# Performance work log

Hardware: AMD Instinct MI355X
Metric: run time of the kernel (lower is better)

The kernel has to match this reference:

```python
import jax, jax.numpy as jnp
import numpy as np
import math

N_HEADS = 12
EPS = 1e-5

def _layernorm(x, w, b):
    # torch .var() is unbiased (ddof=1)
    mean = jnp.mean(x, axis=-1, keepdims=True)
    var = jnp.var(x, axis=-1, keepdims=True, ddof=1)
    return (x - mean) / jnp.sqrt(var + EPS) * w + b

def _gelu_tanh(x):
    c = math.sqrt(2.0 / math.pi)
    return 0.5 * x * (1.0 + jnp.tanh(c * (x + 0.044715 * x * x * x)))

def setup_inputs() -> dict:
    key = jax.random.key(0)
    ks = jax.random.split(key, 6)
    B, T, C = 4, 2048, 768
    s = 0.02
    return {
        "x": jax.random.normal(ks[0], (B, T, C), jnp.float32),
        "ln1_w": jnp.ones((C,), jnp.float32),
        "ln1_b": jnp.zeros((C,), jnp.float32),
        "c_attn_w": jax.random.normal(ks[1], (C, 3 * C), jnp.float32) * s,
        "c_attn_b": jnp.zeros((3 * C,), jnp.float32),
        "c_proj_w": jax.random.normal(ks[2], (C, C), jnp.float32) * s,
        "c_proj_b": jnp.zeros((C,), jnp.float32),
        "ln2_w": jnp.ones((C,), jnp.float32),
        "ln2_b": jnp.zeros((C,), jnp.float32),
        "fc_w": jax.random.normal(ks[3], (C, 4 * C), jnp.float32) * s,
        "fc_b": jnp.zeros((4 * C,), jnp.float32),
        "mproj_w": jax.random.normal(ks[4], (4 * C, C), jnp.float32) * s,
        "mproj_b": jnp.zeros((C,), jnp.float32),
    }

def _attention(x, c_attn_w, c_attn_b, c_proj_w, c_proj_b):
    B, T, C = x.shape
    H = N_HEADS
    D = C // H
    qkv = x @ c_attn_w + c_attn_b  # [B,T,3C]
    q, k, v = jnp.split(qkv, 3, axis=-1)
    q = q.reshape(B, T, H, D).transpose(0, 2, 1, 3)  # [B,H,T,D]
    k = k.reshape(B, T, H, D).transpose(0, 2, 1, 3)
    v = v.reshape(B, T, H, D).transpose(0, 2, 1, 3)
    scores = jnp.einsum("bhqd,bhkd->bhqk", q, k) * (D ** -0.5)  # [B,H,T,T]
    causal = jnp.tril(jnp.ones((T, T), bool))
    scores = jnp.where(causal[None, None], scores, jnp.float32(-jnp.inf))
    attn = jax.nn.softmax(scores, axis=-1)
    out = jnp.einsum("bhqk,bhkd->bhqd", attn, v)  # [B,H,T,D]
    out = out.transpose(0, 2, 1, 3).reshape(B, T, C)
    return out @ c_proj_w + c_proj_b

def reference(x, ln1_w, ln1_b, c_attn_w, c_attn_b, c_proj_w, c_proj_b,
              ln2_w, ln2_b, fc_w, fc_b, mproj_w, mproj_b):
    x = x + _attention(_layernorm(x, ln1_w, ln1_b), c_attn_w, c_attn_b, c_proj_w, c_proj_b)
    h = _gelu_tanh(_layernorm(x, ln2_w, ln2_b) @ fc_w + fc_b)
    return x + h @ mproj_w + mproj_b
```

## Files before the change

### kernel.cpp

```cpp
#include <hip/hip_runtime.h>
#include <hip/hip_bf16.h>
#include <cstdint>

#define BF __hip_bfloat16

typedef __bf16 v8bf __attribute__((ext_vector_type(8)));
typedef float  v4f  __attribute__((ext_vector_type(4)));

__device__ __forceinline__ float tof(BF v) { return __bfloat162float(v); }
__device__ __forceinline__ BF    tob(float v) { return __float2bfloat16(v); }
__device__ __forceinline__ float ldf(float v) { return v; }
__device__ __forceinline__ float ldf(BF v) { return tof(v); }
__device__ __forceinline__ void stv(float* p, float v) { *p = v; }
__device__ __forceinline__ void stv(BF* p, float v) { *p = tob(v); }

__device__ __forceinline__ v4f mfma16(v8bf a, v8bf b, v4f c) {
  return __builtin_amdgcn_mfma_f32_16x16x32_bf16(a, b, c, 0, 0, 0);
}

__device__ __forceinline__ void async16(const BF* g, BF* l) {
  __builtin_amdgcn_global_load_lds((const __attribute__((address_space(1))) void*)g,
                                   (__attribute__((address_space(3))) void*)l, 16, 0, 0);
}

__global__ __launch_bounds__(256) void transpose_k(const float* __restrict__ in,
                                                   BF* __restrict__ out, int R, int C) {
  __shared__ BF t[64][65];
  int tid = threadIdx.x;
  int c0 = blockIdx.x * 64, r0 = blockIdx.y * 64;
#pragma unroll
  for (int i = 0; i < 16; ++i) {
    int idx = i * 256 + tid;
    int rr = idx >> 6, cc = idx & 63;
    t[rr][cc] = tob(in[(size_t)(r0 + rr) * C + c0 + cc]);
  }
  __syncthreads();
#pragma unroll
  for (int i = 0; i < 16; ++i) {
    int idx = i * 256 + tid;
    int rr = idx >> 6, cc = idx & 63;
    out[(size_t)(c0 + rr) * R + r0 + cc] = t[cc][rr];
  }
}

__global__ __launch_bounds__(256) void vtrans_k(const BF* __restrict__ qkv,
                                                BF* __restrict__ vT) {
  __shared__ BF t[64][65];
  int tid = threadIdx.x;
  int t0 = blockIdx.x * 64;
  int bh = blockIdx.y;
  int b = bh / 12, h = bh % 12;
  const BF* src = qkv + (size_t)(b * 2048 + t0) * 2304 + 1536 + h * 64;
#pragma unroll
  for (int i = 0; i < 16; ++i) {
    int idx = i * 256 + tid;
    int rr = idx >> 6, cc = idx & 63;
    t[rr][cc] = src[(size_t)rr * 2304 + cc];
  }
  __syncthreads();
  BF* dst = vT + (size_t)bh * 64 * 2048 + t0;
#pragma unroll
  for (int i = 0; i < 16; ++i) {
    int idx = i * 256 + tid;
    int rr = idx >> 6, cc = idx & 63;
    dst[(size_t)rr * 2048 + cc] = t[cc][rr];
  }
}

template <typename TX>
__global__ __launch_bounds__(256) void ln_k(const TX* __restrict__ x,
                                            const float* __restrict__ w,
                                            const float* __restrict__ bia,
                                            BF* __restrict__ y) {
  int row = blockIdx.x, tid = threadIdx.x;
  const TX* xr = x + (size_t)row * 768;
  float v0 = ldf(xr[tid]), v1 = ldf(xr[tid + 256]), v2 = ldf(xr[tid + 512]);
  float s1 = v0 + v1 + v2;
  float s2 = v0 * v0 + v1 * v1 + v2 * v2;
#pragma unroll
  for (int m = 32; m; m >>= 1) { s1 += __shfl_xor(s1, m); s2 += __shfl_xor(s2, m); }
  __shared__ float rs[4][2];
  int wv = tid >> 6;
  if ((tid & 63) == 0) { rs[wv][0] = s1; rs[wv][1] = s2; }
  __syncthreads();
  s1 = rs[0][0] + rs[1][0] + rs[2][0] + rs[3][0];
  s2 = rs[0][1] + rs[1][1] + rs[2][1] + rs[3][1];
  float mean = s1 * (1.0f / 768.0f);
  float var = fmaxf((s2 - s1 * mean) * (1.0f / 767.0f), 0.0f);
  float rstd = rsqrtf(var + 1e-5f);
  BF* yr = y + (size_t)row * 768;
  yr[tid]       = tob((v0 - mean) * rstd * w[tid]       + bia[tid]);
  yr[tid + 256] = tob((v1 - mean) * rstd * w[tid + 256] + bia[tid + 256]);
  yr[tid + 512] = tob((v2 - mean) * rstd * w[tid + 512] + bia[tid + 512]);
}

__device__ __forceinline__ float gelu_f(float x) {
  float u = 0.7978845608028654f * (x + 0.044715f * x * x * x);
  float e = exp2f(2.8853900817779268f * u);
  return 0.5f * x * (1.0f + (1.0f - 2.0f / (e + 1.0f)));
}

template <int BN, int ACT, bool RESID, typename TR, typename TO>
__global__ __launch_bounds__(256) void gemm_bt_k(
    const BF* __restrict__ A, const BF* __restrict__ Bt, const float* __restrict__ bias,
    const TR* __restrict__ resid, TO* __restrict__ out, int M, int N, int K) {
  constexpr int NW = BN / 32;
  __shared__ __align__(16) BF As[2][128 * 64];
  __shared__ __align__(16) BF Bs[2][BN * 64];
  const int tid = threadIdx.x;
  const int w = tid >> 6, lane = tid & 63;
  const int quad = lane >> 4, l16 = lane & 15;
  const int gx = gridDim.x;
  const int nwg = gx * gridDim.y;
  const int lid = blockIdx.y * gx + blockIdx.x;
  const int swz = (lid & 7) * (nwg >> 3) + (lid >> 3);
  const int m0 = (swz / gx) * 128, n0 = (swz % gx) * BN;
  const int wm = (w >> 1) * 64, wn = (w & 1) * (BN / 2);
  const int sr = lane >> 3;
  const int sc = ((lane & 7) ^ sr) * 8;

  v4f acc[4][NW];
#pragma unroll
  for (int i = 0; i < 4; ++i)
#pragma unroll
    for (int j = 0; j < NW; ++j) acc[i][j] = (v4f){0.f, 0.f, 0.f, 0.f};

  auto stage = [&](int bsel, int k0) {
#pragma unroll
    for (int i = 0; i < 4; ++i) {
      int r0 = w * 32 + i * 8;
      async16(A + (size_t)(m0 + r0 + sr) * K + k0 + sc, &As[bsel][r0 * 64]);
    }
    if (BN == 128) {
#pragma unroll
      for (int i = 0; i < 4; ++i) {
        int r0 = w * 32 + i * 8;
        async16(Bt + (size_t)(n0 + r0 + sr) * K + k0 + sc, &Bs[bsel][r0 * 64]);
      }
    } else {
#pragma unroll
      for (int i = 0; i < 2; ++i) {
        int r0 = w * 16 + i * 8;
        async16(Bt + (size_t)(n0 + r0 + sr) * K + k0 + sc, &Bs[bsel][r0 * 64]);
      }
    }
  };

  const int nkt = K >> 6;
  stage(0, 0);
  __syncthreads();
  for (int kt = 0; kt < nkt; ++kt) {
    const int cur = kt & 1;
    if (kt + 1 < nkt) stage(cur ^ 1, (kt + 1) << 6);
#pragma unroll
    for (int kk = 0; kk < 2; ++kk) {
      v8bf af[4], bfv[NW];
#pragma unroll
      for (int mi = 0; mi < 4; ++mi) {
        int row = wm + mi * 16 + l16;
        af[mi] = *(const v8bf*)&As[cur][row * 64 + (((kk * 4 + quad) ^ (row & 7)) * 8)];
      }
#pragma unroll
      for (int nj = 0; nj < NW; ++nj) {
        int row = wn + nj * 16 + l16;
        bfv[nj] = *(const v8bf*)&Bs[cur][row * 64 + (((kk * 4 + quad) ^ (row & 7)) * 8)];
      }
      __builtin_amdgcn_s_setprio(1);
#pragma unroll
      for (int mi = 0; mi < 4; ++mi)
#pragma unroll
        for (int nj = 0; nj < NW; ++nj)
          acc[mi][nj] = mfma16(af[mi], bfv[nj], acc[mi][nj]);
      __builtin_amdgcn_s_setprio(0);
    }
    __syncthreads();
  }

#pragma unroll
  for (int nj = 0; nj < NW; ++nj) {
    int col = n0 + wn + nj * 16 + l16;
    float bv = bias[col];
#pragma unroll
    for (int mi = 0; mi < 4; ++mi) {
      v4f c = acc[mi][nj];
#pragma unroll
      for (int r = 0; r < 4; ++r) {
        int row = m0 + wm + mi * 16 + quad * 4 + r;
        float v = c[r] + bv;
        if (RESID) v += ldf(resid[(size_t)row * N + col]);
        if (ACT == 1) v = gelu_f(v);
        stv(&out[(size_t)row * N + col], v);
      }
    }
  }
}

__global__ __launch_bounds__(256) void attn_k(const BF* __restrict__ qkv,
                                              const BF* __restrict__ vT,
                                              BF* __restrict__ out) {
  __shared__ __align__(16) BF Ks[64 * 64];
  __shared__ __align__(16) BF Vs[64 * 64];
  __shared__ __align__(16) BF Ps[4][16 * 64];
  const int tid = threadIdx.x;
  const int w = tid >> 6, lane = tid & 63;
  const int quad = lane >> 4, l16 = lane & 15;
  const int bid = blockIdx.x;
  const int qi = 31 - (bid / 48);
  const int bh = bid % 48;
  const int b = bh / 12, h = bh % 12;
  const int q0 = qi * 64;
  const int qf = q0 + w * 16;
  BF* Pw = &Ps[w][0];
  const float L2E = 1.4426950408889634f;

  auto sz = [](int r, int c) { return (r << 6) + (c ^ ((r & 7) << 3)); };

  const BF* qp = qkv + (size_t)(b * 2048 + qf + l16) * 2304 + h * 64;
  v8bf q0v = *(const v8bf*)(qp + quad * 8);
  v8bf q1v = *(const v8bf*)(qp + 32 + quad * 8);
#pragma unroll
  for (int i = 0; i < 8; ++i) {
    q0v[i] = (__bf16)(tof((BF)q0v[i]) * 0.125f);
    q1v[i] = (__bf16)(tof((BF)q1v[i]) * 0.125f);
  }
  v8bf ones;
#pragma unroll
  for (int i = 0; i < 8; ++i) ones[i] = (__bf16)1.0f;

  v4f O[4], S;
#pragma unroll
  for (int j = 0; j < 4; ++j) O[j] = (v4f){0.f, 0.f, 0.f, 0.f};
  S = (v4f){0.f, 0.f, 0.f, 0.f};

  const BF* kg = qkv + (size_t)b * 2048 * 2304 + 768 + h * 64;
  const BF* vg = vT + (size_t)bh * 64 * 2048;
  const int r0 = tid >> 3, c0 = (tid & 7) * 8;
  const int r1 = r0 + 32;
  const int nIter = qi + 1;

  v8bf nk0 = *(const v8bf*)(kg + (size_t)r0 * 2304 + c0);
  v8bf nk1 = *(const v8bf*)(kg + (size_t)r1 * 2304 + c0);
  v8bf nv0 = *(const v8bf*)(vg + (size_t)r0 * 2048 + c0);
  v8bf nv1 = *(const v8bf*)(vg + (size_t)r1 * 2048 + c0);

  for (int t = 0; t < nIter; ++t) {
    const int kt0 = t * 64;
    __syncthreads();
    *(v8bf*)&Ks[sz(r0, c0)] = nk0;
    *(v8bf*)&Ks[sz(r1, c0)] = nk1;
    *(v8bf*)&Vs[sz(r0, c0)] = nv0;
    *(v8bf*)&Vs[sz(r1, c0)] = nv1;
    __syncthreads();
    if (t + 1 < nIter) {
      const int kn = kt0 + 64;
      nk0 = *(const v8bf*)(kg + (size_t)(kn + r0) * 2304 + c0);
      nk1 = *(const v8bf*)(kg + (size_t)(kn + r1) * 2304 + c0);
      nv0 = *(const v8bf*)(vg + (size_t)r0 * 2048 + kn + c0);
      nv1 = *(const v8bf*)(vg + (size_t)r1 * 2048 + kn + c0);
    }
    v4f s[4];
    __builtin_amdgcn_s_setprio(1);
#pragma unroll
    for (int nt = 0; nt < 4; ++nt) {
      v8bf kf0 = *(const v8bf*)&Ks[sz(nt * 16 + l16, quad * 8)];
      v8bf kf1 = *(const v8bf*)&Ks[sz(nt * 16 + l16, 32 + quad * 8)];
      s[nt] = mfma16(q1v, kf1, mfma16(q0v, kf0, (v4f){0.f, 0.f, 0.f, 0.f}));
    }
    __builtin_amdgcn_s_setprio(0);
    if (t < qi) {
#pragma unroll
      for (int nt = 0; nt < 4; ++nt)
#pragma unroll
        for (int r = 0; r < 4; ++r)
          Pw[sz(quad * 4 + r, nt * 16 + l16)] = tob(exp2f(s[nt][r] * L2E));
    } else {
#pragma unroll
      for (int nt = 0; nt < 4; ++nt) {
        int key = kt0 + nt * 16 + l16;
#pragma unroll
        for (int r = 0; r < 4; ++r) {
          int qrow = qf + quad * 4 + r;
          float p = (key <= qrow) ? exp2f(s[nt][r] * L2E) : 0.f;
          Pw[sz(quad * 4 + r, nt * 16 + l16)] = tob(p);
        }
      }
    }
    asm volatile("s_waitcnt lgkmcnt(0)" ::: "memory");
    v8bf p0 = *(const v8bf*)&Pw[sz(l16, quad * 8)];
    v8bf p1 = *(const v8bf*)&Pw[sz(l16, 32 + quad * 8)];
    __builtin_amdgcn_s_setprio(1);
#pragma unroll
    for (int j = 0; j < 4; ++j) {
      v8bf vf0 = *(const v8bf*)&Vs[sz(j * 16 + l16, quad * 8)];
      v8bf vf1 = *(const v8bf*)&Vs[sz(j * 16 + l16, 32 + quad * 8)];
      O[j] = mfma16(p1, vf1, mfma16(p0, vf0, O[j]));
    }
    S = mfma16(p1, ones, mfma16(p0, ones, S));
    __builtin_amdgcn_s_setprio(0);
  }

#pragma unroll
  for (int r = 0; r < 4; ++r) {
    float inv = 1.0f / S[r];
    int row = b * 2048 + qf + quad * 4 + r;
    BF* op = out + (size_t)row * 768 + h * 64 + l16;
#pragma unroll
    for (int j = 0; j < 4; ++j) op[j * 16] = tob(O[j][r] * inv);
  }
}

extern "C" void kernel_launch(void* const* d_in, const int* in_sizes, int n_in,
                              void* d_out, int out_size, void* d_ws, size_t ws_size,
                              hipStream_t stream) {
  const float* x        = (const float*)d_in[0];
  const float* ln1_w    = (const float*)d_in[1];
  const float* ln1_b    = (const float*)d_in[2];
  const float* c_attn_w = (const float*)d_in[3];
  const float* c_attn_b = (const float*)d_in[4];
  const float* c_proj_w = (const float*)d_in[5];
  const float* c_proj_b = (const float*)d_in[6];
  const float* ln2_w    = (const float*)d_in[7];
  const float* ln2_b    = (const float*)d_in[8];
  const float* fc_w     = (const float*)d_in[9];
  const float* fc_b     = (const float*)d_in[10];
  const float* mproj_w  = (const float*)d_in[11];
  const float* mproj_b  = (const float*)d_in[12];
  float* out = (float*)d_out;
  char* wsb = (char*)d_ws;
  dim3 blk(256);

  BF* vT = (BF*)((char*)d_out + 12582912);

  const size_t NEED_BIG = 89653248;
  if (ws_size >= NEED_BIG) {
    BF* qkv      = (BF*)(wsb);
    BF* hbuf     = (BF*)(wsb);
    BF* x2       = (BF*)(wsb + 50331648);
    BF* wT_attn  = (BF*)(wsb + 62914560);
    BF* wT_proj  = (BF*)(wsb + 66453504);
    BF* wT_fc    = (BF*)(wsb + 67633152);
    BF* wT_mproj = (BF*)(wsb + 72351744);
    BF* lnbuf    = (BF*)(wsb + 77070336);
    BF* attnout  = (BF*)d_out;

    transpose_k<<<dim3(36, 12), blk, 0, stream>>>(c_attn_w, wT_attn, 768, 2304);
    transpose_k<<<dim3(12, 12), blk, 0, stream>>>(c_proj_w, wT_proj, 768, 768);
    transpose_k<<<dim3(48, 12), blk, 0, stream>>>(fc_w, wT_fc, 768, 3072);
    transpose_k<<<dim3(12, 48), blk, 0, stream>>>(mproj_w, wT_mproj, 3072, 768);

    ln_k<float><<<8192, blk, 0, stream>>>(x, ln1_w, ln1_b, lnbuf);
    gemm_bt_k<128, 0, false, float, BF><<<dim3(18, 64), blk, 0, stream>>>(
        lnbuf, wT_attn, c_attn_b, (const float*)nullptr, qkv, 8192, 2304, 768);
    vtrans_k<<<dim3(32, 48), blk, 0, stream>>>(qkv, vT);
    attn_k<<<dim3(1536), blk, 0, stream>>>(qkv, vT, attnout);
    gemm_bt_k<64, 0, true, float, BF><<<dim3(12, 64), blk, 0, stream>>>(
        attnout, wT_proj, c_proj_b, x, x2, 8192, 768, 768);
    ln_k<BF><<<8192, blk, 0, stream>>>(x2, ln2_w, ln2_b, lnbuf);
    gemm_bt_k<128, 1, false, float, BF><<<dim3(24, 64), blk, 0, stream>>>(
        lnbuf, wT_fc, fc_b, (const float*)nullptr, hbuf, 8192, 3072, 768);
    gemm_bt_k<64, 0, true, BF, float><<<dim3(12, 64), blk, 0, stream>>>(
        hbuf, wT_mproj, mproj_b, x2, out, 8192, 768, 3072);
  } else {
    BF* ws       = (BF*)d_ws;
    BF* qkv      = ws;
    BF* attnout  = ws + (size_t)18874368;
    BF* wT_attn  = attnout;
    BF* x2       = ws;
    BF* wT_proj  = ws + (size_t)6291456;
    BF* wT_fc    = ws + (size_t)6881280;
    BF* wT_mproj = ws + (size_t)9240576;
    BF* hbuf     = ws + (size_t)11599872;
    BF* lnbuf    = (BF*)d_out;

    transpose_k<<<dim3(36, 12), blk, 0, stream>>>(c_attn_w, wT_attn, 768, 2304);
    ln_k<float><<<8192, blk, 0, stream>>>(x, ln1_w, ln1_b, lnbuf);
    gemm_bt_k<128, 0, false, float, BF><<<dim3(18, 64), blk, 0, stream>>>(
        lnbuf, wT_attn, c_attn_b, (const float*)nullptr, qkv, 8192, 2304, 768);
    vtrans_k<<<dim3(32, 48), blk, 0, stream>>>(qkv, vT);
    attn_k<<<dim3(1536), blk, 0, stream>>>(qkv, vT, attnout);
    transpose_k<<<dim3(12, 12), blk, 0, stream>>>(c_proj_w, wT_proj, 768, 768);
    gemm_bt_k<64, 0, true, float, BF><<<dim3(12, 64), blk, 0, stream>>>(
        attnout, wT_proj, c_proj_b, x, x2, 8192, 768, 768);
    ln_k<BF><<<8192, blk, 0, stream>>>(x2, ln2_w, ln2_b, lnbuf);
    transpose_k<<<dim3(48, 12), blk, 0, stream>>>(fc_w, wT_fc, 768, 3072);
    transpose_k<<<dim3(12, 48), blk, 0, stream>>>(mproj_w, wT_mproj, 3072, 768);
    for (int half = 1; half >= 0; --half) {
      size_t r0 = (size_t)half * 4096;
      gemm_bt_k<128, 1, false, float, BF><<<dim3(24, 32), blk, 0, stream>>>(
          lnbuf + r0 * 768, wT_fc, fc_b, (const float*)nullptr, hbuf, 4096, 3072, 768);
      gemm_bt_k<64, 0, true, BF, float><<<dim3(12, 32), blk, 0, stream>>>(
          hbuf, wT_mproj, mproj_b, x2 + r0 * 768, out + r0 * 768, 4096, 768, 3072);
    }
  }
}
```

Before: 368.5 us.

## Enlarge GEMM tiles to 256x128 with 512 threads and triple-buffered LDS pipeline

Replaces the templated 128xBN GEMM with a single 256x128 tile kernel run by 512 threads (8 waves, each computing 64x64). LDS staging moves from double to triple buffering: two K-tiles are prefetched ahead, and explicit vmcnt waits with raw barriers replace __syncthreads. All fragments for both k-substeps are loaded before the MFMA block. The goal is more data reuse per tile and deeper latency hiding. The cost is larger LDS use (144KB) and fewer workgroups, e.g. 192 for the N=768 GEMMs, which may underfill the CUs.

```diff
diff --git a/kernel.cpp b/kernel.cpp
--- a/kernel.cpp
+++ b/kernel.cpp
@@ -100,13 +100,12 @@
   return 0.5f * x * (1.0f + (1.0f - 2.0f / (e + 1.0f)));
 }
 
-template <int BN, int ACT, bool RESID, typename TR, typename TO>
-__global__ __launch_bounds__(256) void gemm_bt_k(
+template <int ACT, bool RESID, typename TR, typename TO>
+__global__ __launch_bounds__(512) void gemm_bt_k(
     const BF* __restrict__ A, const BF* __restrict__ Bt, const float* __restrict__ bias,
     const TR* __restrict__ resid, TO* __restrict__ out, int M, int N, int K) {
-  constexpr int NW = BN / 32;
-  __shared__ __align__(16) BF As[2][128 * 64];
-  __shared__ __align__(16) BF Bs[2][BN * 64];
+  __shared__ __align__(16) BF As[3 * 256 * 64];
+  __shared__ __align__(16) BF Bs[3 * 128 * 64];
   const int tid = threadIdx.x;
   const int w = tid >> 6, lane = tid & 63;
   const int quad = lane >> 4, l16 = lane & 15;
@@ -114,70 +113,75 @@
   const int nwg = gx * gridDim.y;
   const int lid = blockIdx.y * gx + blockIdx.x;
   const int swz = (lid & 7) * (nwg >> 3) + (lid >> 3);
-  const int m0 = (swz / gx) * 128, n0 = (swz % gx) * BN;
-  const int wm = (w >> 1) * 64, wn = (w & 1) * (BN / 2);
+  const int m0 = (swz / gx) * 256, n0 = (swz % gx) * 128;
+  const int wm = (w >> 1) * 64, wn = (w & 1) * 64;
   const int sr = lane >> 3;
   const int sc = ((lane & 7) ^ sr) * 8;
 
-  v4f acc[4][NW];
+  v4f acc[4][4];
 #pragma unroll
   for (int i = 0; i < 4; ++i)
 #pragma unroll
-    for (int j = 0; j < NW; ++j) acc[i][j] = (v4f){0.f, 0.f, 0.f, 0.f};
-
-  auto stage = [&](int bsel, int k0) {
+    for (int j = 0; j < 4; ++j) acc[i][j] = (v4f){0.f, 0.f, 0.f, 0.f};
+
+  auto stage = [&](int bsel, int kt) {
+    const int k0 = kt << 6;
+    BF* Ab = As + bsel * (256 * 64);
+    BF* Bb = Bs + bsel * (128 * 64);
 #pragma unroll
     for (int i = 0; i < 4; ++i) {
       int r0 = w * 32 + i * 8;
-      async16(A + (size_t)(m0 + r0 + sr) * K + k0 + sc, &As[bsel][r0 * 64]);
-    }
-    if (BN == 128) {
-#pragma unroll
-      for (int i = 0; i < 4; ++i) {
-        int r0 = w * 32 + i * 8;
-        async16(Bt + (size_t)(n0 + r0 + sr) * K + k0 + sc, &Bs[bsel][r0 * 64]);
-      }
-    } else {
-#pragma unroll
-      for (int i = 0; i < 2; ++i) {
-        int r0 = w * 16 + i * 8;
-        async16(Bt + (size_t)(n0 + r0 + sr) * K + k0 + sc, &Bs[bsel][r0 * 64]);
-      }
+      async16(A + (size_t)(m0 + r0 + sr) * K + k0 + sc, Ab + r0 * 64);
+    }
+#pragma unroll
+    for (int i = 0; i < 2; ++i) {
+      int r0 = w * 16 + i * 8;
+      async16(Bt + (size_t)(n0 + r0 + sr) * K + k0 + sc, Bb + r0 * 64);
     }
   };
 
   const int nkt = K >> 6;
   stage(0, 0);
-  __syncthreads();
+  stage(1, 1);
+  asm volatile("s_waitcnt vmcnt(6)" ::: "memory");
+  __builtin_amdgcn_s_barrier();
+
   for (int kt = 0; kt < nkt; ++kt) {
-    const int cur = kt & 1;
-    if (kt + 1 < nkt) stage(cur ^ 1, (kt + 1) << 6);
+    if (kt + 2 < nkt) stage((kt + 2) % 3, kt + 2);
+    const BF* Ab = As + (kt % 3) * (256 * 64);
+    const BF* Bb = Bs + (kt % 3) * (128 * 64);
+    v8bf af[2][4], bfv[2][4];
 #pragma unroll
     for (int kk = 0; kk < 2; ++kk) {
-      v8bf af[4], bfv[NW];
 #pragma unroll
       for (int mi = 0; mi < 4; ++mi) {
         int row = wm + mi * 16 + l16;
-        af[mi] = *(const v8bf*)&As[cur][row * 64 + (((kk * 4 + quad) ^ (row & 7)) * 8)];
+        af[kk][mi] = *(const v8bf*)&Ab[row * 64 + (((kk * 4 + quad) ^ (row & 7)) * 8)];
       }
 #pragma unroll
-      for (int nj = 0; nj < NW; ++nj) {
+      for (int nj = 0; nj < 4; ++nj) {
         int row = wn + nj * 16 + l16;
-        bfv[nj] = *(const v8bf*)&Bs[cur][row * 64 + (((kk * 4 + quad) ^ (row & 7)) * 8)];
+        bfv[kk][nj] = *(const v8bf*)&Bb[row * 64 + (((kk * 4 + quad) ^ (row & 7)) * 8)];
       }
-      __builtin_amdgcn_s_setprio(1);
+    }
+    __builtin_amdgcn_s_setprio(1);
+#pragma unroll
+    for (int kk = 0; kk < 2; ++kk)
 #pragma unroll
       for (int mi = 0; mi < 4; ++mi)
 #pragma unroll
-        for (int nj = 0; nj < NW; ++nj)
-          acc[mi][nj] = mfma16(af[mi], bfv[nj], acc[mi][nj]);
-      __builtin_amdgcn_s_setprio(0);
-    }
-    __syncthreads();
-  }
-
-#pragma unroll
-  for (int nj = 0; nj < NW; ++nj) {
+        for (int nj = 0; nj < 4; ++nj)
+          acc[mi][nj] = mfma16(af[kk][mi], bfv[kk][nj], acc[mi][nj]);
+    __builtin_amdgcn_s_setprio(0);
+    if (kt + 1 < nkt) {
+      if (kt + 2 < nkt) asm volatile("s_waitcnt vmcnt(6)" ::: "memory");
+      else              asm volatile("s_waitcnt vmcnt(0)" ::: "memory");
+      __builtin_amdgcn_s_barrier();
+    }
+  }
+
+#pragma unroll
+  for (int nj = 0; nj < 4; ++nj) {
     int col = n0 + wn + nj * 16 + l16;
     float bv = bias[col];
 #pragma unroll
@@ -328,6 +332,7 @@
   float* out = (float*)d_out;
   char* wsb = (char*)d_ws;
   dim3 blk(256);
+  dim3 blk2(512);
 
   BF* vT = (BF*)((char*)d_out + 12582912);
 
@@ -349,16 +354,16 @@
     transpose_k<<<dim3(12, 48), blk, 0, stream>>>(mproj_w, wT_mproj, 3072, 768);
 
     ln_k<float><<<8192, blk, 0, stream>>>(x, ln1_w, ln1_b, lnbuf);
-    gemm_bt_k<128, 0, false, float, BF><<<dim3(18, 64), blk, 0, stream>>>(
+    gemm_bt_k<0, false, float, BF><<<dim3(18, 32), blk2, 0, stream>>>(
         lnbuf, wT_attn, c_attn_b, (const float*)nullptr, qkv, 8192, 2304, 768);
     vtrans_k<<<dim3(32, 48), blk, 0, stream>>>(qkv, vT);
     attn_k<<<dim3(1536), blk, 0, stream>>>(qkv, vT, attnout);
-    gemm_bt_k<64, 0, true, float, BF><<<dim3(12, 64), blk, 0, stream>>>(
+    gemm_bt_k<0, true, float, BF><<<dim3(6, 32), blk2, 0, stream>>>(
         attnout, wT_proj, c_proj_b, x, x2, 8192, 768, 768);
     ln_k<BF><<<8192, blk, 0, stream>>>(x2, ln2_w, ln2_b, lnbuf);
-    gemm_bt_k<128, 1, false, float, BF><<<dim3(24, 64), blk, 0, stream>>>(
+    gemm_bt_k<1, false, float, BF><<<dim3(24, 32), blk2, 0, stream>>>(
         lnbuf, wT_fc, fc_b, (const float*)nullptr, hbuf, 8192, 3072, 768);
-    gemm_bt_k<64, 0, true, BF, float><<<dim3(12, 64), blk, 0, stream>>>(
+    gemm_bt_k<0, true, BF, float><<<dim3(6, 32), blk2, 0, stream>>>(
         hbuf, wT_mproj, mproj_b, x2, out, 8192, 768, 3072);
   } else {
     BF* ws       = (BF*)d_ws;
@@ -374,21 +379,21 @@
 
     transpose_k<<<dim3(36, 12), blk, 0, stream>>>(c_attn_w, wT_attn, 768, 2304);
     ln_k<float><<<8192, blk, 0, stream>>>(x, ln1_w, ln1_b, lnbuf);
-    gemm_bt_k<128, 0, false, float, BF><<<dim3(18, 64), blk, 0, stream>>>(
+    gemm_bt_k<0, false, float, BF><<<dim3(18, 32), blk2, 0, stream>>>(
         lnbuf, wT_attn, c_attn_b, (const float*)nullptr, qkv, 8192, 2304, 768);
     vtrans_k<<<dim3(32, 48), blk, 0, stream>>>(qkv, vT);
     attn_k<<<dim3(1536), blk, 0, stream>>>(qkv, vT, attnout);
     transpose_k<<<dim3(12, 12), blk, 0, stream>>>(c_proj_w, wT_proj, 768, 768);
-    gemm_bt_k<64, 0, true, float, BF><<<dim3(12, 64), blk, 0, stream>>>(
+    gemm_bt_k<0, true, float, BF><<<dim3(6, 32), blk2, 0, stream>>>(
         attnout, wT_proj, c_proj_b, x, x2, 8192, 768, 768);
     ln_k<BF><<<8192, blk, 0, stream>>>(x2, ln2_w, ln2_b, lnbuf);
     transpose_k<<<dim3(48, 12), blk, 0, stream>>>(fc_w, wT_fc, 768, 3072);
     transpose_k<<<dim3(12, 48), blk, 0, stream>>>(mproj_w, wT_mproj, 3072, 768);
     for (int half = 1; half >= 0; --half) {
       size_t r0 = (size_t)half * 4096;
-      gemm_bt_k<128, 1, false, float, BF><<<dim3(24, 32), blk, 0, stream>>>(
+      gemm_bt_k<1, false, float, BF><<<dim3(24, 16), blk2, 0, stream>>>(
           lnbuf + r0 * 768, wT_fc, fc_b, (const float*)nullptr, hbuf, 4096, 3072, 768);
-      gemm_bt_k<64, 0, true, BF, float><<<dim3(12, 32), blk, 0, stream>>>(
+      gemm_bt_k<0, true, BF, float><<<dim3(6, 16), blk2, 0, stream>>>(
           hbuf, wT_mproj, mproj_b, x2 + r0 * 768, out + r0 * 768, 4096, 768, 3072);
     }
   }
```

Result: slower. 411.5 us (+11.7%).

## Add 256x256-tile 512-thread GEMM kernel for QKV and FC projections

Applied to the files above, without the earlier changes.

Adds a new GEMM kernel with 256x256 output tiles, 8 waves per block, and a split staging schedule. B and A tiles are loaded asynchronously at different barriers, overlapping with MFMA work on the current k-slice. It replaces the 128-row kernel for the wide QKV and FC GEMMs to raise arithmetic intensity and cut redundant global/LDS traffic. The cost is much larger LDS use (128KB per block) and higher register pressure, and the grids are small (288 or 384 blocks), so CU utilisation may suffer.

```diff
diff --git a/kernel.cpp b/kernel.cpp
--- a/kernel.cpp
+++ b/kernel.cpp
@@ -101,7 +101,7 @@
 }
 
 template <int BN, int ACT, bool RESID, typename TR, typename TO>
-__global__ __launch_bounds__(256) void gemm_bt_k(
+__global__ __launch_bounds__(256) void gemm_sm_k(
     const BF* __restrict__ A, const BF* __restrict__ Bt, const float* __restrict__ bias,
     const TR* __restrict__ resid, TO* __restrict__ out, int M, int N, int K) {
   constexpr int NW = BN / 32;
@@ -186,6 +186,153 @@
 #pragma unroll
       for (int r = 0; r < 4; ++r) {
         int row = m0 + wm + mi * 16 + quad * 4 + r;
+        float v = c[r] + bv;
+        if (RESID) v += ldf(resid[(size_t)row * N + col]);
+        if (ACT == 1) v = gelu_f(v);
+        stv(&out[(size_t)row * N + col], v);
+      }
+    }
+  }
+}
+
+template <int ACT, bool RESID, typename TR, typename TO>
+__global__ __launch_bounds__(512, 2) void gemm256_k(
+    const BF* __restrict__ A, const BF* __restrict__ Bt, const float* __restrict__ bias,
+    const TR* __restrict__ resid, TO* __restrict__ out, int M, int N, int K) {
+  __shared__ __align__(16) BF As[2][256 * 64];
+  __shared__ __align__(16) BF Bs[2][256 * 64];
+  const int tid = threadIdx.x;
+  const int w = tid >> 6, lane = tid & 63;
+  const int quad = lane >> 4, l16 = lane & 15;
+  const int wr = w >> 2, wc = w & 3;
+  const int gx = gridDim.x;
+  const int nwg = gx * gridDim.y;
+  const int lid = blockIdx.y * gx + blockIdx.x;
+  const int swz = (lid & 7) * (nwg >> 3) + (lid >> 3);
+  const int m0 = (swz / gx) * 256, n0 = (swz % gx) * 256;
+  const int srow = tid >> 3;
+  const int scol = ((tid & 7) ^ (srow & 7)) * 8;
+  const int lwb = (w * 8) * 64;
+
+  v4f acc[8][4];
+#pragma unroll
+  for (int i = 0; i < 8; ++i)
+#pragma unroll
+    for (int j = 0; j < 4; ++j) acc[i][j] = (v4f){0.f, 0.f, 0.f, 0.f};
+
+  auto stageB = [&](int bsel, int kt) {
+    const int k0 = kt << 6;
+#pragma unroll
+    for (int i = 0; i < 4; ++i)
+      async16(Bt + (size_t)(n0 + i * 64 + srow) * K + k0 + scol,
+              &Bs[bsel][i * 64 * 64 + lwb]);
+  };
+  auto stageA = [&](int bsel, int kt) {
+    const int k0 = kt << 6;
+#pragma unroll
+    for (int i = 0; i < 4; ++i)
+      async16(A + (size_t)(m0 + i * 64 + srow) * K + k0 + scol,
+              &As[bsel][i * 64 * 64 + lwb]);
+  };
+
+  const int nkt = K >> 6;
+  stageB(0, 0);
+  stageA(0, 0);
+
+  for (int kt = 0; kt < nkt; ++kt) {
+    const int cur = kt & 1;
+    const BF* Ab = As[cur];
+    const BF* Bb = Bs[cur];
+    asm volatile("s_waitcnt vmcnt(1)" ::: "memory");
+    __builtin_amdgcn_s_barrier();
+    asm volatile("" ::: "memory");
+    if (kt + 1 < nkt) stageB(cur ^ 1, kt + 1);
+    v8bf b0[4], a0[4];
+#pragma unroll
+    for (int nj = 0; nj < 4; ++nj) {
+      int r = wc * 64 + nj * 16 + l16;
+      b0[nj] = *(const v8bf*)&Bb[r * 64 + ((quad ^ (r & 7)) * 8)];
+    }
+#pragma unroll
+    for (int mi = 0; mi < 4; ++mi) {
+      int r = wr * 128 + mi * 16 + l16;
+      a0[mi] = *(const v8bf*)&Ab[r * 64 + ((quad ^ (r & 7)) * 8)];
+    }
+    __builtin_amdgcn_s_setprio(1);
+#pragma unroll
+    for (int mi = 0; mi < 4; ++mi)
+#pragma unroll
+      for (int nj = 0; nj < 4; ++nj)
+        acc[mi][nj] = mfma16(a0[mi], b0[nj], acc[mi][nj]);
+    __builtin_amdgcn_s_setprio(0);
+    if (kt + 1 < nkt) asm volatile("s_waitcnt vmcnt(4)" ::: "memory");
+    else              asm volatile("s_waitcnt vmcnt(0)" ::: "memory");
+    __builtin_amdgcn_s_barrier();
+    asm volatile("" ::: "memory");
+    if (kt + 1 < nkt) stageA(cur ^ 1, kt + 1);
+    {
+      v8bf a1[4];
+#pragma unroll
+      for (int mi = 0; mi < 4; ++mi) {
+        int r = wr * 128 + (mi + 4) * 16 + l16;
+        a1[mi] = *(const v8bf*)&Ab[r * 64 + ((quad ^ (r & 7)) * 8)];
+      }
+      __builtin_amdgcn_s_setprio(1);
+#pragma unroll
+      for (int mi = 0; mi < 4; ++mi)
+#pragma unroll
+        for (int nj = 0; nj < 4; ++nj)
+          acc[mi + 4][nj] = mfma16(a1[mi], b0[nj], acc[mi + 4][nj]);
+      __builtin_amdgcn_s_setprio(0);
+    }
+    v8bf b1[4];
+    {
+      v8bf a2[4];
+#pragma unroll
+      for (int nj = 0; nj < 4; ++nj) {
+        int r = wc * 64 + nj * 16 + l16;
+        b1[nj] = *(const v8bf*)&Bb[r * 64 + (((4 + quad) ^ (r & 7)) * 8)];
+      }
+#pragma unroll
+      for (int mi = 0; mi < 4; ++mi) {
+        int r = wr * 128 + mi * 16 + l16;
+        a2[mi] = *(const v8bf*)&Ab[r * 64 + (((4 + quad) ^ (r & 7)) * 8)];
+      }
+      __builtin_amdgcn_s_setprio(1);
+#pragma unroll
+      for (int mi = 0; mi < 4; ++mi)
+#pragma unroll
+        for (int nj = 0; nj < 4; ++nj)
+          acc[mi][nj] = mfma16(a2[mi], b1[nj], acc[mi][nj]);
+      __builtin_amdgcn_s_setprio(0);
+    }
+    {
+      v8bf a3[4];
+#pragma unroll
+      for (int mi = 0; mi < 4; ++mi) {
+        int r = wr * 128 + (mi + 4) * 16 + l16;
+        a3[mi] = *(const v8bf*)&Ab[r * 64 + (((4 + quad) ^ (r & 7)) * 8)];
+      }
+      __builtin_amdgcn_s_setprio(1);
+#pragma unroll
+      for (int mi = 0; mi < 4; ++mi)
+#pragma unroll
+        for (int nj = 0; nj < 4; ++nj)
+          acc[mi + 4][nj] = mfma16(a3[mi], b1[nj], acc[mi + 4][nj]);
+      __builtin_amdgcn_s_setprio(0);
+    }
+  }
+
+#pragma unroll
+  for (int nj = 0; nj < 4; ++nj) {
+    int col = n0 + wc * 64 + nj * 16 + l16;
+    float bv = bias[col];
+#pragma unroll
+    for (int mi = 0; mi < 8; ++mi) {
+      v4f c = acc[mi][nj];
+#pragma unroll
+      for (int r = 0; r < 4; ++r) {
+        int row = m0 + wr * 128 + mi * 16 + quad * 4 + r;
         float v = c[r] + bv;
         if (RESID) v += ldf(resid[(size_t)row * N + col]);
         if (ACT == 1) v = gelu_f(v);
@@ -328,6 +475,7 @@
   float* out = (float*)d_out;
   char* wsb = (char*)d_ws;
   dim3 blk(256);
+  dim3 blk2(512);
 
   BF* vT = (BF*)((char*)d_out + 12582912);
 
@@ -349,16 +497,16 @@
     transpose_k<<<dim3(12, 48), blk, 0, stream>>>(mproj_w, wT_mproj, 3072, 768);
 
     ln_k<float><<<8192, blk, 0, stream>>>(x, ln1_w, ln1_b, lnbuf);
-    gemm_bt_k<128, 0, false, float, BF><<<dim3(18, 64), blk, 0, stream>>>(
+    gemm256_k<0, false, float, BF><<<dim3(9, 32), blk2, 0, stream>>>(
         lnbuf, wT_attn, c_attn_b, (const float*)nullptr, qkv, 8192, 2304, 768);
     vtrans_k<<<dim3(32, 48), blk, 0, stream>>>(qkv, vT);
     attn_k<<<dim3(1536), blk, 0, stream>>>(qkv, vT, attnout);
-    gemm_bt_k<64, 0, true, float, BF><<<dim3(12, 64), blk, 0, stream>>>(
+    gemm_sm_k<64, 0, true, float, BF><<<dim3(12, 64), blk, 0, stream>>>(
         attnout, wT_proj, c_proj_b, x, x2, 8192, 768, 768);
     ln_k<BF><<<8192, blk, 0, stream>>>(x2, ln2_w, ln2_b, lnbuf);
-    gemm_bt_k<128, 1, false, float, BF><<<dim3(24, 64), blk, 0, stream>>>(
+    gemm256_k<1, false, float, BF><<<dim3(12, 32), blk2, 0, stream>>>(
         lnbuf, wT_fc, fc_b, (const float*)nullptr, hbuf, 8192, 3072, 768);
-    gemm_bt_k<64, 0, true, BF, float><<<dim3(12, 64), blk, 0, stream>>>(
+    gemm_sm_k<64, 0, true, BF, float><<<dim3(12, 64), blk, 0, stream>>>(
         hbuf, wT_mproj, mproj_b, x2, out, 8192, 768, 3072);
   } else {
     BF* ws       = (BF*)d_ws;
@@ -374,21 +522,21 @@
 
     transpose_k<<<dim3(36, 12), blk, 0, stream>>>(c_attn_w, wT_attn, 768, 2304);
     ln_k<float><<<8192, blk, 0, stream>>>(x, ln1_w, ln1_b, lnbuf);
-    gemm_bt_k<128, 0, false, float, BF><<<dim3(18, 64), blk, 0, stream>>>(
+    gemm256_k<0, false, float, BF><<<dim3(9, 32), blk2, 0, stream>>>(
         lnbuf, wT_attn, c_attn_b, (const float*)nullptr, qkv, 8192, 2304, 768);
     vtrans_k<<<dim3(32, 48), blk, 0, stream>>>(qkv, vT);
     attn_k<<<dim3(1536), blk, 0, stream>>>(qkv, vT, attnout);
     transpose_k<<<dim3(12, 12), blk, 0, stream>>>(c_proj_w, wT_proj, 768, 768);
-    gemm_bt_k<64, 0, true, float, BF><<<dim3(12, 64), blk, 0, stream>>>(
+    gemm_sm_k<64, 0, true, float, BF><<<dim3(12, 64), blk, 0, stream>>>(
         attnout, wT_proj, c_proj_b, x, x2, 8192, 768, 768);
     ln_k<BF><<<8192, blk, 0, stream>>>(x2, ln2_w, ln2_b, lnbuf);
     transpose_k<<<dim3(48, 12), blk, 0, stream>>>(fc_w, wT_fc, 768, 3072);
     transpose_k<<<dim3(12, 48), blk, 0, stream>>>(mproj_w, wT_mproj, 3072, 768);
     for (int half = 1; half >= 0; --half) {
       size_t r0 = (size_t)half * 4096;
-      gemm_bt_k<128, 1, false, float, BF><<<dim3(24, 32), blk, 0, stream>>>(
+      gemm256_k<1, false, float, BF><<<dim3(12, 16), blk2, 0, stream>>>(
           lnbuf + r0 * 768, wT_fc, fc_b, (const float*)nullptr, hbuf, 4096, 3072, 768);
-      gemm_bt_k<64, 0, true, BF, float><<<dim3(12, 32), blk, 0, stream>>>(
+      gemm_sm_k<64, 0, true, BF, float><<<dim3(12, 32), blk, 0, stream>>>(
           hbuf, wT_mproj, mproj_b, x2 + r0 * 768, out + r0 * 768, 4096, 768, 3072);
     }
   }
```

After: 408.5 us. +10.9%, slower.

## Add triple-buffered GEMM kernel and fuse weight transposes with first layernorm

Applied to the files above, without the earlier changes.

Adds a new GEMM kernel with a 128x64 tile and a three-stage async global-to-LDS pipeline. Waits use explicit vmcnt counts and a single barrier per k-step, so loads run two tiles ahead of compute. The kernel replaces the QKV, c_proj and mproj GEMMs, and the QKV GEMM now launches twice as many narrower tiles. The four weight transposes and the first layernorm are merged into one prep kernel to cut launch count. The costs are more LDS per block, which may lower occupancy, and less B-tile reuse on the QKV GEMM.

```diff
diff --git a/kernel.cpp b/kernel.cpp
--- a/kernel.cpp
+++ b/kernel.cpp
@@ -40,6 +40,60 @@
     int idx = i * 256 + tid;
     int rr = idx >> 6, cc = idx & 63;
     out[(size_t)(c0 + rr) * R + r0 + cc] = t[cc][rr];
+  }
+}
+
+__global__ __launch_bounds__(256) void prep_k(
+    const float* __restrict__ caw, BF* __restrict__ oca,
+    const float* __restrict__ pw,  BF* __restrict__ opj,
+    const float* __restrict__ fw,  BF* __restrict__ ofc,
+    const float* __restrict__ mw,  BF* __restrict__ omp,
+    const float* __restrict__ x, const float* __restrict__ lw,
+    const float* __restrict__ lb, BF* __restrict__ y) {
+  __shared__ BF t[64][65];
+  __shared__ float rs[4][2];
+  const int bid = blockIdx.x;
+  const int tid = threadIdx.x;
+  if (bid < 1728) {
+    const float* in; BF* out; int R, C, bx, by;
+    if (bid < 432)       { in = caw; out = oca; R = 768;  C = 2304; bx = bid % 36; by = bid / 36; }
+    else if (bid < 576)  { int i = bid - 432;  in = pw; out = opj; R = 768;  C = 768;  bx = i % 12; by = i / 12; }
+    else if (bid < 1152) { int i = bid - 576;  in = fw; out = ofc; R = 768;  C = 3072; bx = i % 48; by = i / 48; }
+    else                 { int i = bid - 1152; in = mw; out = omp; R = 3072; C = 768;  bx = i % 12; by = i / 12; }
+    int c0 = bx * 64, r0 = by * 64;
+#pragma unroll
+    for (int i = 0; i < 16; ++i) {
+      int idx = i * 256 + tid;
+      int rr = idx >> 6, cc = idx & 63;
+      t[rr][cc] = tob(in[(size_t)(r0 + rr) * C + c0 + cc]);
+    }
+    __syncthreads();
+#pragma unroll
+    for (int i = 0; i < 16; ++i) {
+      int idx = i * 256 + tid;
+      int rr = idx >> 6, cc = idx & 63;
+      out[(size_t)(c0 + rr) * R + r0 + cc] = t[cc][rr];
+    }
+  } else {
+    int row = bid - 1728;
+    const float* xr = x + (size_t)row * 768;
+    float v0 = xr[tid], v1 = xr[tid + 256], v2 = xr[tid + 512];
+    float s1 = v0 + v1 + v2;
+    float s2 = v0 * v0 + v1 * v1 + v2 * v2;
+#pragma unroll
+    for (int m = 32; m; m >>= 1) { s1 += __shfl_xor(s1, m); s2 += __shfl_xor(s2, m); }
+    int wv = tid >> 6;
+    if ((tid & 63) == 0) { rs[wv][0] = s1; rs[wv][1] = s2; }
+    __syncthreads();
+    s1 = rs[0][0] + rs[1][0] + rs[2][0] + rs[3][0];
+    s2 = rs[0][1] + rs[1][1] + rs[2][1] + rs[3][1];
+    float mean = s1 * (1.0f / 768.0f);
+    float var = fmaxf((s2 - s1 * mean) * (1.0f / 767.0f), 0.0f);
+    float rstd = rsqrtf(var + 1e-5f);
+    BF* yr = y + (size_t)row * 768;
+    yr[tid]       = tob((v0 - mean) * rstd * lw[tid]       + lb[tid]);
+    yr[tid + 256] = tob((v1 - mean) * rstd * lw[tid + 256] + lb[tid + 256]);
+    yr[tid + 512] = tob((v2 - mean) * rstd * lw[tid + 512] + lb[tid + 512]);
   }
 }
 
@@ -101,7 +155,7 @@
 }
 
 template <int BN, int ACT, bool RESID, typename TR, typename TO>
-__global__ __launch_bounds__(256) void gemm_bt_k(
+__global__ __launch_bounds__(256) void gemm_sm_k(
     const BF* __restrict__ A, const BF* __restrict__ Bt, const float* __restrict__ bias,
     const TR* __restrict__ resid, TO* __restrict__ out, int M, int N, int K) {
   constexpr int NW = BN / 32;
@@ -178,6 +232,103 @@
 
 #pragma unroll
   for (int nj = 0; nj < NW; ++nj) {
+    int col = n0 + wn + nj * 16 + l16;
+    float bv = bias[col];
+#pragma unroll
+    for (int mi = 0; mi < 4; ++mi) {
+      v4f c = acc[mi][nj];
+#pragma unroll
+      for (int r = 0; r < 4; ++r) {
+        int row = m0 + wm + mi * 16 + quad * 4 + r;
+        float v = c[r] + bv;
+        if (RESID) v += ldf(resid[(size_t)row * N + col]);
+        if (ACT == 1) v = gelu_f(v);
+        stv(&out[(size_t)row * N + col], v);
+      }
+    }
+  }
+}
+
+template <int ACT, bool RESID, typename TR, typename TO>
+__global__ __launch_bounds__(256) void gemm3_k(
+    const BF* __restrict__ A, const BF* __restrict__ Bt, const float* __restrict__ bias,
+    const TR* __restrict__ resid, TO* __restrict__ out, int M, int N, int K) {
+  __shared__ __align__(16) BF As[3][128 * 64];
+  __shared__ __align__(16) BF Bs[3][64 * 64];
+  const int tid = threadIdx.x;
+  const int w = tid >> 6, lane = tid & 63;
+  const int quad = lane >> 4, l16 = lane & 15;
+  const int gx = gridDim.x;
+  const int nwg = gx * gridDim.y;
+  const int lid = blockIdx.y * gx + blockIdx.x;
+  const int swz = (lid & 7) * (nwg >> 3) + (lid >> 3);
+  const int m0 = (swz / gx) * 128, n0 = (swz % gx) * 64;
+  const int wm = (w >> 1) * 64, wn = (w & 1) * 32;
+  const int sr = lane >> 3;
+  const int sc = ((lane & 7) ^ sr) * 8;
+
+  v4f acc[4][2];
+#pragma unroll
+  for (int i = 0; i < 4; ++i)
+#pragma unroll
+    for (int j = 0; j < 2; ++j) acc[i][j] = (v4f){0.f, 0.f, 0.f, 0.f};
+
+  auto stage = [&](int bsel, int kt) {
+    const int k0 = kt << 6;
+#pragma unroll
+    for (int i = 0; i < 4; ++i) {
+      int r0 = w * 32 + i * 8;
+      async16(A + (size_t)(m0 + r0 + sr) * K + k0 + sc, &As[bsel][r0 * 64]);
+    }
+#pragma unroll
+    for (int i = 0; i < 2; ++i) {
+      int r0 = w * 16 + i * 8;
+      async16(Bt + (size_t)(n0 + r0 + sr) * K + k0 + sc, &Bs[bsel][r0 * 64]);
+    }
+  };
+
+  const int nkt = K >> 6;
+  stage(0, 0);
+  stage(1, 1);
+  asm volatile("s_waitcnt vmcnt(6)" ::: "memory");
+  __builtin_amdgcn_s_barrier();
+  asm volatile("" ::: "memory");
+
+  for (int kt = 0; kt < nkt; ++kt) {
+    if (kt + 2 < nkt) stage((kt + 2) % 3, kt + 2);
+    const BF* Ab = As[kt % 3];
+    const BF* Bb = Bs[kt % 3];
+#pragma unroll
+    for (int kk = 0; kk < 2; ++kk) {
+      v8bf af[4], bfv[2];
+#pragma unroll
+      for (int mi = 0; mi < 4; ++mi) {
+        int row = wm + mi * 16 + l16;
+        af[mi] = *(const v8bf*)&Ab[row * 64 + (((kk * 4 + quad) ^ (row & 7)) * 8)];
+      }
+#pragma unroll
+      for (int nj = 0; nj < 2; ++nj) {
+        int row = wn + nj * 16 + l16;
+        bfv[nj] = *(const v8bf*)&Bb[row * 64 + (((kk * 4 + quad) ^ (row & 7)) * 8)];
+      }
+      __builtin_amdgcn_s_setprio(1);
+#pragma unroll
+      for (int mi = 0; mi < 4; ++mi)
+#pragma unroll
+        for (int nj = 0; nj < 2; ++nj)
+          acc[mi][nj] = mfma16(af[mi], bfv[nj], acc[mi][nj]);
+      __builtin_amdgcn_s_setprio(0);
+    }
+    if (kt + 1 < nkt) {
+      if (kt + 2 < nkt) asm volatile("s_waitcnt vmcnt(6)" ::: "memory");
+      else              asm volatile("s_waitcnt vmcnt(0)" ::: "memory");
+      __builtin_amdgcn_s_barrier();
+      asm volatile("" ::: "memory");
+    }
+  }
+
+#pragma unroll
+  for (int nj = 0; nj < 2; ++nj) {
     int col = n0 + wn + nj * 16 + l16;
     float bv = bias[col];
 #pragma unroll
@@ -343,22 +494,19 @@
     BF* lnbuf    = (BF*)(wsb + 77070336);
     BF* attnout  = (BF*)d_out;
 
-    transpose_k<<<dim3(36, 12), blk, 0, stream>>>(c_attn_w, wT_attn, 768, 2304);
-    transpose_k<<<dim3(12, 12), blk, 0, stream>>>(c_proj_w, wT_proj, 768, 768);
-    transpose_k<<<dim3(48, 12), blk, 0, stream>>>(fc_w, wT_fc, 768, 3072);
-    transpose_k<<<dim3(12, 48), blk, 0, stream>>>(mproj_w, wT_mproj, 3072, 768);
-
-    ln_k<float><<<8192, blk, 0, stream>>>(x, ln1_w, ln1_b, lnbuf);
-    gemm_bt_k<128, 0, false, float, BF><<<dim3(18, 64), blk, 0, stream>>>(
+    prep_k<<<dim3(9920), blk, 0, stream>>>(c_attn_w, wT_attn, c_proj_w, wT_proj,
+                                           fc_w, wT_fc, mproj_w, wT_mproj,
+                                           x, ln1_w, ln1_b, lnbuf);
+    gemm3_k<0, false, float, BF><<<dim3(36, 64), blk, 0, stream>>>(
         lnbuf, wT_attn, c_attn_b, (const float*)nullptr, qkv, 8192, 2304, 768);
     vtrans_k<<<dim3(32, 48), blk, 0, stream>>>(qkv, vT);
     attn_k<<<dim3(1536), blk, 0, stream>>>(qkv, vT, attnout);
-    gemm_bt_k<64, 0, true, float, BF><<<dim3(12, 64), blk, 0, stream>>>(
+    gemm3_k<0, true, float, BF><<<dim3(12, 64), blk, 0, stream>>>(
         attnout, wT_proj, c_proj_b, x, x2, 8192, 768, 768);
     ln_k<BF><<<8192, blk, 0, stream>>>(x2, ln2_w, ln2_b, lnbuf);
-    gemm_bt_k<128, 1, false, float, BF><<<dim3(24, 64), blk, 0, stream>>>(
+    gemm_sm_k<128, 1, false, float, BF><<<dim3(24, 64), blk, 0, stream>>>(
         lnbuf, wT_fc, fc_b, (const float*)nullptr, hbuf, 8192, 3072, 768);
-    gemm_bt_k<64, 0, true, BF, float><<<dim3(12, 64), blk, 0, stream>>>(
+    gemm3_k<0, true, BF, float><<<dim3(12, 64), blk, 0, stream>>>(
         hbuf, wT_mproj, mproj_b, x2, out, 8192, 768, 3072);
   } else {
     BF* ws       = (BF*)d_ws;
@@ -374,21 +522,21 @@
 
     transpose_k<<<dim3(36, 12), blk, 0, stream>>>(c_attn_w, wT_attn, 768, 2304);
     ln_k<float><<<8192, blk, 0, stream>>>(x, ln1_w, ln1_b, lnbuf);
-    gemm_bt_k<128, 0, false, float, BF><<<dim3(18, 64), blk, 0, stream>>>(
+    gemm3_k<0, false, float, BF><<<dim3(36, 64), blk, 0, stream>>>(
         lnbuf, wT_attn, c_attn_b, (const float*)nullptr, qkv, 8192, 2304, 768);
     vtrans_k<<<dim3(32, 48), blk, 0, stream>>>(qkv, vT);
     attn_k<<<dim3(1536), blk, 0, stream>>>(qkv, vT, attnout);
     transpose_k<<<dim3(12, 12), blk, 0, stream>>>(c_proj_w, wT_proj, 768, 768);
-    gemm_bt_k<64, 0, true, float, BF><<<dim3(12, 64), blk, 0, stream>>>(
+    gemm3_k<0, true, float, BF><<<dim3(12, 64), blk, 0, stream>>>(
         attnout, wT_proj, c_proj_b, x, x2, 8192, 768, 768);
     ln_k<BF><<<8192, blk, 0, stream>>>(x2, ln2_w, ln2_b, lnbuf);
     transpose_k<<<dim3(48, 12), blk, 0, stream>>>(fc_w, wT_fc, 768, 3072);
     transpose_k<<<dim3(12, 48), blk, 0, stream>>>(mproj_w, wT_mproj, 3072, 768);
     for (int half = 1; half >= 0; --half) {
       size_t r0 = (size_t)half * 4096;
-      gemm_bt_k<128, 1, false, float, BF><<<dim3(24, 32), blk, 0, stream>>>(
+      gemm_sm_k<128, 1, false, float, BF><<<dim3(24, 32), blk, 0, stream>>>(
           lnbuf + r0 * 768, wT_fc, fc_b, (const float*)nullptr, hbuf, 4096, 3072, 768);
-      gemm_bt_k<64, 0, true, BF, float><<<dim3(12, 32), blk, 0, stream>>>(
+      gemm3_k<0, true, BF, float><<<dim3(12, 32), blk, 0, stream>>>(
           hbuf, wT_mproj, mproj_b, x2 + r0 * 768, out + r0 * 768, 4096, 768, 3072);
     }
   }
```

New measurement: 416.1 us. 12.9% more time.
